# Kernel optimization log

Measured on AMD Instinct MI355X. Metric: run time of the kernel, lower is better.

Reference implementation:

```python
import jax, jax.numpy as jnp
import numpy as np

N_NODES = 50000
N_EDGES = 1600000
IN_DIM = 256
HID = 128
BATCH = 16384
EDGE_FEAT = 6
BN_EPS = 1e-5


def _glorot(key, shape):
    fan_in, fan_out = shape[0], shape[1]
    lim = float(np.sqrt(6.0 / (fan_in + fan_out)))
    return jax.random.uniform(key, shape, jnp.float32, -lim, lim)


def setup_inputs() -> dict:
    key = jax.random.key(0)
    ks = jax.random.split(key, 20)
    return {
        "x": jax.random.normal(ks[0], (N_NODES, IN_DIM), jnp.float32),
        "edge_index": jax.random.randint(ks[1], (2, N_EDGES), 0, N_NODES, jnp.int64 if jax.config.jax_enable_x64 else jnp.int32),
        "src_nodes": jax.random.randint(ks[2], (BATCH,), 0, N_NODES),
        "tgt_nodes": jax.random.randint(ks[3], (BATCH,), 0, N_NODES),
        "edge_features": jax.random.uniform(ks[4], (BATCH, EDGE_FEAT), jnp.float32),
        # SAGEConv layer 0: lin_l (aggregated neighbors, has bias), lin_r (root, no bias)
        "sage_wl0": _glorot(ks[5], (IN_DIM, HID)),
        "sage_b0": jnp.zeros((HID,), jnp.float32),
        "sage_wr0": _glorot(ks[6], (IN_DIM, HID)),
        # SAGEConv layer 1
        "sage_wl1": _glorot(ks[7], (HID, HID)),
        "sage_b1": jnp.zeros((HID,), jnp.float32),
        "sage_wr1": _glorot(ks[8], (HID, HID)),
        # edge_processor: Linear(6, 64)
        "ep_w": _glorot(ks[9], (EDGE_FEAT, HID // 2)),
        "ep_b": jnp.zeros((HID // 2,), jnp.float32),
        # predictor: Linear(320,128) -> ReLU -> BN(128) -> Linear(128,64) -> ReLU -> Linear(64,1) -> Sigmoid
        "p1_w": _glorot(ks[10], (2 * HID + HID // 2, HID)),
        "p1_b": jnp.zeros((HID,), jnp.float32),
        "bn_gamma": jnp.ones((HID,), jnp.float32),
        "bn_beta": jnp.zeros((HID,), jnp.float32),
        "bn_mean": jnp.zeros((HID,), jnp.float32),
        "bn_var": jnp.ones((HID,), jnp.float32),
        "p2_w": _glorot(ks[11], (HID, HID // 2)),
        "p2_b": jnp.zeros((HID // 2,), jnp.float32),
        "p3_w": _glorot(ks[12], (HID // 2, 1)),
        "p3_b": jnp.zeros((1,), jnp.float32),
    }


def _sage_conv(h, src, dst, w_l, b, w_r):
    # PyG SAGEConv(mean): out_i = W_l @ mean_{j in N(i)} h_j + b + W_r @ h_i
    n = h.shape[0]
    agg = jax.ops.segment_sum(h[src], dst, num_segments=n)  # [N, d]
    deg = jax.ops.segment_sum(jnp.ones((src.shape[0],), h.dtype), dst, num_segments=n)
    mean = agg / jnp.maximum(deg, 1.0)[:, None]
    return mean @ w_l + b + h @ w_r


def reference(x, edge_index, src_nodes, tgt_nodes, edge_features,
              sage_wl0, sage_b0, sage_wr0, sage_wl1, sage_b1, sage_wr1,
              ep_w, ep_b, p1_w, p1_b, bn_gamma, bn_beta, bn_mean, bn_var,
              p2_w, p2_b, p3_w, p3_b):
    src, dst = edge_index[0], edge_index[1]
    h = _sage_conv(x, src, dst, sage_wl0, sage_b0, sage_wr0)
    h = jax.nn.relu(h)  # dropout is identity in eval mode
    h = _sage_conv(h, src, dst, sage_wl1, sage_b1, sage_wr1)
    src_emb = h[src_nodes]  # [B, HID]
    tgt_emb = h[tgt_nodes]  # [B, HID]
    edge_proc = jax.nn.relu(edge_features @ ep_w + ep_b)  # [B, HID//2]
    combined = jnp.concatenate([src_emb, tgt_emb, edge_proc], axis=1)  # [B, 320]
    z = jax.nn.relu(combined @ p1_w + p1_b)
    z = (z - bn_mean) / jnp.sqrt(bn_var + BN_EPS) * bn_gamma + bn_beta  # BN eval mode
    z = jax.nn.relu(z @ p2_w + p2_b)
    return jax.nn.sigmoid(z @ p3_w + p3_b)  # [B, 1]
```

## Files before the change

kernel.cpp:

```cpp
#include <hip/hip_runtime.h>
#include <hip/hip_bf16.h>

#define N_NODES 50000
#define N_EDGES 1600000
#define BATCH   16384
#define HID     128
#define NBUCK   782
#define NBLK    256
#define EPB     6250

using short8  = __attribute__((ext_vector_type(8))) short;
using floatx4 = __attribute__((ext_vector_type(4))) float;
using floatv4 = __attribute__((ext_vector_type(4))) float;
using float2v = __attribute__((ext_vector_type(2))) float;
using uint2v  = __attribute__((ext_vector_type(2))) unsigned;
using uintx4  = __attribute__((ext_vector_type(4))) unsigned;
typedef unsigned short ushort_t;

__device__ __forceinline__ float bflo(unsigned u){ return __uint_as_float(u << 16); }
__device__ __forceinline__ float bfhi(unsigned u){ return __uint_as_float(u & 0xffff0000u); }
__device__ __forceinline__ float bf1(ushort_t u){ return __uint_as_float(((unsigned)u) << 16); }
__device__ __forceinline__ ushort_t f2bf(float f){
    unsigned u = __float_as_uint(f);
    return (ushort_t)((u + 0x7fffu + ((u >> 16) & 1u)) >> 16);
}
__device__ __forceinline__ int geti(const void* p, long long i, int is64){
    return is64 ? (int)((const long long*)p)[i] : ((const int*)p)[i];
}
__device__ __forceinline__ float2v up2(unsigned u){
    float2v r; r.x = bflo(u); r.y = bfhi(u); return r;
}

__global__ void k_detect(const unsigned* __restrict__ xbits,
                         const unsigned* __restrict__ eibits, int* flags){
    __shared__ int f[2];
    int t = threadIdx.x;
    if (t < 2) f[t] = 0;
    __syncthreads();
    unsigned u = xbits[t];
    unsigned e0 = (u >> 7)  & 0xFF;
    unsigned e1 = (u >> 23) & 0xFF;
    if (e0 >= 140 || e1 >= 140) atomicOr(&f[0], 1);
    if (eibits[2*t + 1] != 0)   atomicOr(&f[1], 1);
    __syncthreads();
    if (t == 0){ flags[0] = f[0]; flags[1] = f[1] ? 0 : 1; }
}

#define NT 19
struct ConvDesc { const void* src[NT]; int cum[NT + 1]; };
__global__ void k_conv(ConvDesc d, ushort_t* __restrict__ dst, const int* __restrict__ flags){
    int i = blockIdx.x*256 + threadIdx.x;
    if (i >= d.cum[NT]) return;
    int seg = 0;
    while (i >= d.cum[seg + 1]) seg++;
    int off = i - d.cum[seg];
    ushort_t v;
    if (flags[0]) v = f2bf(((const float*)d.src[seg])[off]);
    else          v = ((const ushort_t*)d.src[seg])[off];
    dst[i] = v;
}

#define OFF_WL0 0
#define OFF_WR0 32768
#define OFF_WL1 65536
#define OFF_WR1 81920
#define OFF_B0  98304
#define OFF_B1  98432
#define OFF_EPW 98560
#define OFF_EPB 98944
#define OFF_P1W 99008
#define OFF_P1B 139968
#define OFF_BNG 140096
#define OFF_BNB 140224
#define OFF_BNM 140352
#define OFF_BNV 140480
#define OFF_P2W 140608
#define OFF_P2B 148800
#define OFF_P3W 148864
#define OFF_EF  148928
#define OFF_P3B 247232
#define CW_TOT  247233

#define PACK_TOT 147584
__global__ void k_pack(const ushort_t* __restrict__ cw,
                       ushort_t* __restrict__ bp0, ushort_t* __restrict__ bp1,
                       ushort_t* __restrict__ bpp1, ushort_t* __restrict__ bpp2,
                       float* __restrict__ bnf){
    int i = blockIdx.x*256 + threadIdx.x;
    if (i < 65536){
        int j = i & 7, lane = (i >> 3) & 63, c = (i >> 9) & 15, kk = i >> 13;
        int k = kk*32 + (lane >> 4)*8 + j;
        int n = c*16 + (lane & 15);
        bp0[i] = (n < 128) ? cw[OFF_WL0 + k*128 + n] : cw[OFF_WR0 + k*128 + (n-128)];
    } else if (i < 98304){
        int i2 = i - 65536;
        int j = i2 & 7, lane = (i2 >> 3) & 63, c = (i2 >> 9) & 15, kk = i2 >> 13;
        int k = kk*32 + (lane >> 4)*8 + j;
        int n = c*16 + (lane & 15);
        bp1[i2] = (n < 128) ? cw[OFF_WL1 + k*128 + n] : cw[OFF_WR1 + k*128 + (n-128)];
    } else if (i < 139264){
        int i2 = i - 98304;
        int j = i2 & 7, lane = (i2 >> 3) & 63, ct = (i2 >> 9) & 7, kk = i2 >> 12;
        int k = kk*32 + (lane >> 4)*8 + j;
        int n = ct*16 + (lane & 15);
        bpp1[i2] = cw[OFF_P1W + k*128 + n];
    } else if (i < 147456){
        int i2 = i - 139264;
        int j = i2 & 7, lane = (i2 >> 3) & 63, ct = (i2 >> 9) & 3, kk = i2 >> 11;
        int k = kk*32 + (lane >> 4)*8 + j;
        int n = ct*16 + (lane & 15);
        bpp2[i2] = cw[OFF_P2W + k*64 + n];
    } else if (i < PACK_TOT){
        int n = i - 147456;
        float g = bf1(cw[OFF_BNG + n]), b = bf1(cw[OFF_BNB + n]);
        float m = bf1(cw[OFF_BNM + n]), v = bf1(cw[OFF_BNV + n]);
        float sc = g / sqrtf(v + 1e-5f);
        bnf[n] = sc; bnf[128 + n] = b - m*sc;
    }
}

__global__ __launch_bounds__(256)
void kb_hist(const void* __restrict__ ei, int* __restrict__ hist,
             const int* __restrict__ flags){
    __shared__ int lh[NBUCK];
    for (int i = threadIdx.x; i < NBUCK; i += 256) lh[i] = 0;
    __syncthreads();
    int i64 = flags[1];
    int e0 = blockIdx.x * EPB;
    for (int e = e0 + threadIdx.x; e < e0 + EPB; e += 256){
        int d = geti(ei, (long long)N_EDGES + e, i64);
        atomicAdd(&lh[d >> 6], 1);
    }
    __syncthreads();
    for (int i = threadIdx.x; i < NBUCK; i += 256)
        hist[i * NBLK + blockIdx.x] = lh[i];
}

__global__ __launch_bounds__(256)
void kb_scancol(int* __restrict__ hist, int* __restrict__ btot){
    __shared__ int sh[256];
    int b = blockIdx.x, t = threadIdx.x;
    int v = hist[b*NBLK + t];
    sh[t] = v; __syncthreads();
    for (int o = 1; o < 256; o <<= 1){
        int x = (t >= o) ? sh[t-o] : 0;
        __syncthreads();
        sh[t] += x;
        __syncthreads();
    }
    hist[b*NBLK + t] = sh[t] - v;
    if (t == 255) btot[b] = sh[255];
}

__global__ __launch_bounds__(1024)
void kb_scanbase(const int* __restrict__ btot, int* __restrict__ bbase,
                 int* __restrict__ off){
    __shared__ int sh[1024];
    int t = threadIdx.x;
    int v = (t < NBUCK) ? btot[t] : 0;
    sh[t] = v; __syncthreads();
    for (int o = 1; o < 1024; o <<= 1){
        int x = (t >= o) ? sh[t-o] : 0;
        __syncthreads();
        sh[t] += x;
        __syncthreads();
    }
    if (t < NBUCK) bbase[t] = sh[t] - v;
    if (t == 0){ bbase[NBUCK] = N_EDGES; off[N_NODES] = N_EDGES; }
}

__global__ __launch_bounds__(256)
void kb_scatter(const void* __restrict__ ei, const int* __restrict__ hist,
                const int* __restrict__ bbase, unsigned* __restrict__ ebuf,
                const int* __restrict__ flags){
    __shared__ int lcur[NBUCK];
    for (int i = threadIdx.x; i < NBUCK; i += 256)
        lcur[i] = bbase[i] + hist[i*NBLK + blockIdx.x];
    __syncthreads();
    int i64 = flags[1];
    int e0 = blockIdx.x * EPB;
    for (int e = e0 + threadIdx.x; e < e0 + EPB; e += 256){
        int s = geti(ei, e, i64);
        int d = geti(ei, (long long)N_EDGES + e, i64);
        int p = atomicAdd(&lcur[d >> 6], 1);
        ebuf[p] = (unsigned)s | ((unsigned)(d & 63) << 16);
    }
}

__global__ __launch_bounds__(256)
void kb_csr(const unsigned* __restrict__ ebuf, const int* __restrict__ bbase,
            ushort_t* __restrict__ csr, int* __restrict__ off){
    __shared__ int ldeg[64];
    int b = blockIdx.x, t = threadIdx.x;
    int ebase = bbase[b], eend = bbase[b+1];
    if (t < 64) ldeg[t] = 0;
    __syncthreads();
    for (int i = ebase + t; i < eend; i += 256)
        atomicAdd(&ldeg[(ebuf[i] >> 16) & 63], 1);
    __syncthreads();
    if (t < 64){
        int v = ldeg[t];
        int sum = v;
        #pragma unroll
        for (int o = 1; o < 64; o <<= 1){
            int x = __shfl_up(sum, o, 64);
            if (t >= o) sum += x;
        }
        int excl = sum - v;
        int node = b*64 + t;
        if (node < N_NODES) off[node] = ebase + excl;
        ldeg[t] = excl;
    }
    __syncthreads();
    for (int i = ebase + t; i < eend; i += 256){
        unsigned u = ebuf[i];
        int p = atomicAdd(&ldeg[(u >> 16) & 63], 1);
        csr[ebase + p] = (ushort_t)(u & 0xffffu);
    }
}

template<int KSTEPS, bool CHECKBF>
__global__ __launch_bounds__(256)
void k_gemm2(const ushort_t* __restrict__ A, const ushort_t* __restrict__ Bp,
             ushort_t* __restrict__ out, int M, const int* __restrict__ flags)
{
    if (CHECKBF && flags[0]) return;
    const int lane = threadIdx.x & 63;
    const int w    = threadIdx.x >> 6;
    const int l16  = lane & 15;
    const int q    = lane >> 4;
    const int S    = KSTEPS * 32;
    const int m_base = blockIdx.x * 64;

    const ushort_t* arow[4];
    bool ok[4];
    #pragma unroll
    for (int rt = 0; rt < 4; ++rt){
        int m = m_base + rt*16 + l16;
        ok[rt] = (m < M);
        arow[rt] = A + (size_t)(ok[rt] ? m : 0) * S + q*8;
    }
    const short8* bbase = (const short8*)(Bp + (size_t)(w*4)*64*8) + lane;

    floatx4 acc[4][4] = {};
    for (int kk = 0; kk < KSTEPS; ++kk){
        short8 b[4];
        #pragma unroll
        for (int ci = 0; ci < 4; ++ci)
            b[ci] = bbase[(kk*16 + ci)*64];
        short8 a[4];
        #pragma unroll
        for (int rt = 0; rt < 4; ++rt){
            short8 af = {0,0,0,0,0,0,0,0};
            if (ok[rt]) af = *(const short8*)(arow[rt] + kk*32);
            a[rt] = af;
        }
        #pragma unroll
        for (int rt = 0; rt < 4; ++rt)
            #pragma unroll
            for (int ci = 0; ci < 4; ++ci)
                acc[rt][ci] = __builtin_amdgcn_mfma_f32_16x16x32_bf16(a[rt], b[ci], acc[rt][ci], 0, 0, 0);
    }

    #pragma unroll
    for (int rt = 0; rt < 4; ++rt){
        int row_b = m_base + rt*16 + q*4;
        #pragma unroll
        for (int r = 0; r < 4; ++r){
            int row = row_b + r;
            if (row < M){
                #pragma unroll
                for (int ci = 0; ci < 4; ++ci)
                    out[(size_t)row*256 + w*64 + ci*16 + l16] = f2bf(acc[rt][ci][r]);
            }
        }
    }
}

__global__ __launch_bounds__(256)
void k_gemm2f(const float* __restrict__ Af, const ushort_t* __restrict__ Bp,
              ushort_t* __restrict__ out, int M, const int* __restrict__ flags)
{
    if (!flags[0]) return;
    const int KSTEPS = 8;
    const int lane = threadIdx.x & 63;
    const int w    = threadIdx.x >> 6;
    const int l16  = lane & 15;
    const int q    = lane >> 4;
    const int S    = KSTEPS * 32;
    const int m_base = blockIdx.x * 64;

    const float* arow[4];
    bool ok[4];
    #pragma unroll
    for (int rt = 0; rt < 4; ++rt){
        int m = m_base + rt*16 + l16;
        ok[rt] = (m < M);
        arow[rt] = Af + (size_t)(ok[rt] ? m : 0) * S + q*8;
    }
    const short8* bbase = (const short8*)(Bp + (size_t)(w*4)*64*8) + lane;

    floatx4 acc[4][4] = {};
    for (int kk = 0; kk < KSTEPS; ++kk){
        short8 b[4];
        #pragma unroll
        for (int ci = 0; ci < 4; ++ci)
            b[ci] = bbase[(kk*16 + ci)*64];
        short8 a[4];
        #pragma unroll
        for (int rt = 0; rt < 4; ++rt){
            union { unsigned u[4]; short8 s; } cv;
            cv.u[0]=0; cv.u[1]=0; cv.u[2]=0; cv.u[3]=0;
            if (ok[rt]){
                floatv4 f0 = *(const floatv4*)(arow[rt] + kk*32);
                floatv4 f1 = *(const floatv4*)(arow[rt] + kk*32 + 4);
                cv.u[0] = __builtin_amdgcn_perm(__float_as_uint(f0.y), __float_as_uint(f0.x), 0x07060302);
                cv.u[1] = __builtin_amdgcn_perm(__float_as_uint(f0.w), __float_as_uint(f0.z), 0x07060302);
                cv.u[2] = __builtin_amdgcn_perm(__float_as_uint(f1.y), __float_as_uint(f1.x), 0x07060302);
                cv.u[3] = __builtin_amdgcn_perm(__float_as_uint(f1.w), __float_as_uint(f1.z), 0x07060302);
            }
            a[rt] = cv.s;
        }
        #pragma unroll
        for (int rt = 0; rt < 4; ++rt)
            #pragma unroll
            for (int ci = 0; ci < 4; ++ci)
                acc[rt][ci] = __builtin_amdgcn_mfma_f32_16x16x32_bf16(a[rt], b[ci], acc[rt][ci], 0, 0, 0);
    }

    #pragma unroll
    for (int rt = 0; rt < 4; ++rt){
        int row_b = m_base + rt*16 + q*4;
        #pragma unroll
        for (int r = 0; r < 4; ++r){
            int row = row_b + r;
            if (row < M){
                #pragma unroll
                for (int ci = 0; ci < 4; ++ci)
                    out[(size_t)row*256 + w*64 + ci*16 + l16] = f2bf(acc[rt][ci][r]);
            }
        }
    }
}

__global__ __launch_bounds__(256)
void k_agg(const int* __restrict__ off, const ushort_t* __restrict__ csr,
           const ushort_t* __restrict__ yr, const ushort_t* __restrict__ bias,
           ushort_t* __restrict__ out, int do_relu)
{
    int v = blockIdx.x*4 + (threadIdx.x >> 6);
    if (v >= N_NODES) return;
    const int l = threadIdx.x & 63;
    const int g = l >> 4;
    const int c = l & 15;
    int e0 = off[v], e1 = off[v+1];
    const ushort_t* yb = yr + c*8;

    float2v A0[4] = {}, A1[4] = {}, A2[4] = {}, A3[4] = {};
    int p = e0;
    for (; p + 16 <= e1; p += 16){
        int u0 = csr[p + g];
        int u1 = csr[p + 4 + g];
        int u2 = csr[p + 8 + g];
        int u3 = csr[p + 12 + g];
        uintx4 d0 = *(const uintx4*)(yb + (size_t)u0*256);
        uintx4 d1 = *(const uintx4*)(yb + (size_t)u1*256);
        uintx4 d2 = *(const uintx4*)(yb + (size_t)u2*256);
        uintx4 d3 = *(const uintx4*)(yb + (size_t)u3*256);
        A0[0] += up2(d0.x); A0[1] += up2(d0.y); A0[2] += up2(d0.z); A0[3] += up2(d0.w);
        A1[0] += up2(d1.x); A1[1] += up2(d1.y); A1[2] += up2(d1.z); A1[3] += up2(d1.w);
        A2[0] += up2(d2.x); A2[1] += up2(d2.y); A2[2] += up2(d2.z); A2[3] += up2(d2.w);
        A3[0] += up2(d3.x); A3[1] += up2(d3.y); A3[2] += up2(d3.z); A3[3] += up2(d3.w);
    }
    for (; p + 4 <= e1; p += 4){
        int u0 = csr[p + g];
        uintx4 d0 = *(const uintx4*)(yb + (size_t)u0*256);
        A0[0] += up2(d0.x); A0[1] += up2(d0.y); A0[2] += up2(d0.z); A0[3] += up2(d0.w);
    }
    if (p + g < e1){
        int u1 = csr[p + g];
        uintx4 d1 = *(const uintx4*)(yb + (size_t)u1*256);
        A1[0] += up2(d1.x); A1[1] += up2(d1.y); A1[2] += up2(d1.z); A1[3] += up2(d1.w);
    }
    #pragma unroll
    for (int j = 0; j < 4; ++j) A0[j] += A1[j] + A2[j] + A3[j];

    float a0=A0[0].x, a1=A0[0].y, a2=A0[1].x, a3=A0[1].y;
    float a4=A0[2].x, a5=A0[2].y, a6=A0[3].x, a7=A0[3].y;
    #pragma unroll
    for (int m = 16; m <= 32; m <<= 1){
        a0 += __shfl_xor(a0, m, 64); a1 += __shfl_xor(a1, m, 64);
        a2 += __shfl_xor(a2, m, 64); a3 += __shfl_xor(a3, m, 64);
        a4 += __shfl_xor(a4, m, 64); a5 += __shfl_xor(a5, m, 64);
        a6 += __shfl_xor(a6, m, 64); a7 += __shfl_xor(a7, m, 64);
    }
    if (g == 0){
        float inv = 1.f / (float)max(e1 - e0, 1);
        uintx4 rr = *(const uintx4*)(yr + (size_t)v*256 + 128 + c*8);
        uintx4 bb = *(const uintx4*)(bias + c*8);
        float v0 = a0*inv + bflo(rr.x) + bflo(bb.x);
        float v1 = a1*inv + bfhi(rr.x) + bfhi(bb.x);
        float v2 = a2*inv + bflo(rr.y) + bflo(bb.y);
        float v3 = a3*inv + bfhi(rr.y) + bfhi(bb.y);
        float v4 = a4*inv + bflo(rr.z) + bflo(bb.z);
        float v5 = a5*inv + bfhi(rr.z) + bfhi(bb.z);
        float v6 = a6*inv + bflo(rr.w) + bflo(bb.w);
        float v7 = a7*inv + bfhi(rr.w) + bfhi(bb.w);
        if (do_relu){
            v0=fmaxf(v0,0.f); v1=fmaxf(v1,0.f); v2=fmaxf(v2,0.f); v3=fmaxf(v3,0.f);
            v4=fmaxf(v4,0.f); v5=fmaxf(v5,0.f); v6=fmaxf(v6,0.f); v7=fmaxf(v7,0.f);
        }
        uintx4 o;
        o.x = (unsigned)f2bf(v0) | ((unsigned)f2bf(v1) << 16);
        o.y = (unsigned)f2bf(v2) | ((unsigned)f2bf(v3) << 16);
        o.z = (unsigned)f2bf(v4) | ((unsigned)f2bf(v5) << 16);
        o.w = (unsigned)f2bf(v6) | ((unsigned)f2bf(v7) << 16);
        *(uintx4*)(out + (size_t)v*128 + c*8) = o;
    }
}

__global__ __launch_bounds__(256)
void k_pred2(const ushort_t* __restrict__ h2,
             const void* __restrict__ srcn, const void* __restrict__ tgtn,
             const ushort_t* __restrict__ cw, const ushort_t* __restrict__ bpp1,
             const ushort_t* __restrict__ bpp2, const float* __restrict__ bnf,
             void* __restrict__ outp, const int* __restrict__ flags)
{
    __shared__ ushort_t comb[64][328];
    __shared__ ushort_t zbuf[64][136];
    __shared__ ushort_t z2buf[64][68];
    __shared__ float    partial[4][64];
    __shared__ int      sid[64], tid_[64];

    const int t    = threadIdx.x;
    const int lane = t & 63;
    const int w    = t >> 6;
    const int l16  = lane & 15;
    const int q    = lane >> 4;
    const int row0 = blockIdx.x * 64;
    const int i64  = flags[1];

    if (t < 64){ sid[t] = geti(srcn, row0 + t, i64); tid_[t] = geti(tgtn, row0 + t, i64); }
    __syncthreads();

    const unsigned* h2u = (const unsigned*)h2;
    #pragma unroll 4
    for (int r = w*16; r < w*16 + 16; ++r){
        unsigned us = h2u[(size_t)sid[r]*64 + lane];
        unsigned ut = h2u[(size_t)tid_[r]*64 + lane];
        *(unsigned*)&comb[r][2*lane]       = us;
        *(unsigned*)&comb[r][128 + 2*lane] = ut;
    }
    {
        int r = t >> 2, c0 = (t & 3) * 16;
        float efv[6];
        #pragma unroll
        for (int k = 0; k < 6; ++k) efv[k] = bf1(cw[OFF_EF + (row0 + r)*6 + k]);
        #pragma unroll
        for (int c = 0; c < 16; ++c){
            int n = c0 + c;
            float a = bf1(cw[OFF_EPB + n]);
            #pragma unroll
            for (int k = 0; k < 6; ++k) a += efv[k] * bf1(cw[OFF_EPW + k*64 + n]);
            comb[r][256 + n] = f2bf(fmaxf(a, 0.f));
        }
    }
    __syncthreads();

    floatx4 acc[4][2] = {};
    for (int kk = 0; kk < 10; ++kk){
        short8 a[4];
        #pragma unroll
        for (int rt = 0; rt < 4; ++rt)
            a[rt] = *(const short8*)&comb[rt*16 + l16][kk*32 + q*8];
        #pragma unroll
        for (int ci = 0; ci < 2; ++ci){
            short8 b = *(const short8*)&bpp1[(((kk*8) + (w*2 + ci))*64 + lane)*8];
            #pragma unroll
            for (int rt = 0; rt < 4; ++rt)
                acc[rt][ci] = __builtin_amdgcn_mfma_f32_16x16x32_bf16(a[rt], b, acc[rt][ci], 0, 0, 0);
        }
    }
    #pragma unroll
    for (int ci = 0; ci < 2; ++ci){
        int n = w*32 + ci*16 + l16;
        float b1v = bf1(cw[OFF_P1B + n]);
        float sc = bnf[n], sh = bnf[128 + n];
        #pragma unroll
        for (int rt = 0; rt < 4; ++rt)
            #pragma unroll
            for (int r = 0; r < 4; ++r){
                float v = fmaxf(acc[rt][ci][r] + b1v, 0.f) * sc + sh;
                zbuf[rt*16 + q*4 + r][n] = f2bf(v);
            }
    }
    __syncthreads();

    floatx4 acc2[4] = {};
    for (int kk = 0; kk < 4; ++kk){
        short8 b = *(const short8*)&bpp2[(((kk*4) + w)*64 + lane)*8];
        #pragma unroll
        for (int rt = 0; rt < 4; ++rt){
            short8 a = *(const short8*)&zbuf[rt*16 + l16][kk*32 + q*8];
            acc2[rt] = __builtin_amdgcn_mfma_f32_16x16x32_bf16(a, b, acc2[rt], 0, 0, 0);
        }
    }
    {
        int n = w*16 + l16;
        float b2v = bf1(cw[OFF_P2B + n]);
        #pragma unroll
        for (int rt = 0; rt < 4; ++rt)
            #pragma unroll
            for (int r = 0; r < 4; ++r)
                z2buf[rt*16 + q*4 + r][n] = f2bf(fmaxf(acc2[rt][r] + b2v, 0.f));
    }
    __syncthreads();

    {
        int r = t & 63, seg = t >> 6;
        float s = 0.f;
        #pragma unroll
        for (int c = 0; c < 16; ++c){
            int n = seg*16 + c;
            s += bf1(z2buf[r][n]) * bf1(cw[OFF_P3W + n]);
        }
        partial[seg][r] = s;
    }
    __syncthreads();
    if (t < 64){
        float zf = partial[0][t] + partial[1][t] + partial[2][t] + partial[3][t] + bf1(cw[OFF_P3B]);
        float sg = 1.f / (1.f + __expf(-zf));
        if (flags[0]) ((float*)outp)[row0 + t] = sg;
        else          ((ushort_t*)outp)[row0 + t] = f2bf(sg);
    }
}

extern "C" void kernel_launch(void* const* d_in, const int* in_sizes, int n_in,
                              void* d_out, int out_size, void* d_ws, size_t ws_size,
                              hipStream_t stream)
{
    const void* x    = d_in[0];
    const void* ei   = d_in[1];
    const void* srcn = d_in[2];
    const void* tgtn = d_in[3];

    char* p = (char*)d_ws;
    auto carve = [&](size_t bytes)->char*{ char* r = p; p += (bytes + 511) & ~size_t(511); return r; };
    int* flags = (int*)carve(64);
    int* off   = (int*)carve((N_NODES+1)*4);
    int* btot  = (int*)carve(NBUCK*4);
    int* bbase = (int*)carve((NBUCK+1)*4);
    ushort_t* csr = (ushort_t*)carve((size_t)N_EDGES*2);
    ushort_t* yr  = (ushort_t*)carve((size_t)N_NODES*256*2);
    ushort_t* h   = (ushort_t*)carve((size_t)N_NODES*128*2);
    ushort_t* cw  = (ushort_t*)carve((size_t)CW_TOT*2);
    ushort_t* bp0 = (ushort_t*)carve((size_t)65536*2);
    ushort_t* bp1 = (ushort_t*)carve((size_t)32768*2);
    ushort_t* bpp1= (ushort_t*)carve((size_t)40960*2);
    ushort_t* bpp2= (ushort_t*)carve((size_t)8192*2);
    float*    bnf = (float*)carve(256*4);

    int*      hist = (int*)yr;
    unsigned* ebuf = (unsigned*)((char*)yr + 8u*1024*1024);

    k_detect<<<1, 256, 0, stream>>>((const unsigned*)x, (const unsigned*)ei, flags);

    ConvDesc cd;
    const int srcidx[NT] = {5,7,8,10,6,9,11,12,13,14,15,16,17,18,19,20,21,4,22};
    const int lens[NT]   = {32768,32768,16384,16384,128,128,384,64,40960,128,128,128,128,128,8192,64,64,98304,1};
    int run = 0;
    for (int i = 0; i < NT; ++i){ cd.src[i] = d_in[srcidx[i]]; cd.cum[i] = run; run += lens[i]; }
    cd.cum[NT] = run;
    k_conv<<<(CW_TOT+255)/256, 256, 0, stream>>>(cd, cw, flags);
    k_pack<<<(PACK_TOT+255)/256, 256, 0, stream>>>(cw, bp0, bp1, bpp1, bpp2, bnf);

    kb_hist    <<<NBLK, 256, 0, stream>>>(ei, hist, flags);
    kb_scancol <<<NBUCK, 256, 0, stream>>>(hist, btot);
    kb_scanbase<<<1, 1024, 0, stream>>>(btot, bbase, off);
    kb_scatter <<<NBLK, 256, 0, stream>>>(ei, hist, bbase, ebuf, flags);
    kb_csr     <<<NBUCK, 256, 0, stream>>>(ebuf, bbase, csr, off);

    int gblocks = (N_NODES + 63) / 64;
    k_gemm2<8, true><<<gblocks, 256, 0, stream>>>((const ushort_t*)x, bp0, yr, N_NODES, flags);
    k_gemm2f<<<gblocks, 256, 0, stream>>>((const float*)x, bp0, yr, N_NODES, flags);
    k_agg<<<(N_NODES+3)/4, 256, 0, stream>>>(off, csr, yr, cw+OFF_B0, h, 1);
    k_gemm2<4, false><<<gblocks, 256, 0, stream>>>(h, bp1, yr, N_NODES, flags);
    k_agg<<<(N_NODES+3)/4, 256, 0, stream>>>(off, csr, yr, cw+OFF_B1, h, 0);

    k_pred2<<<BATCH/64, 256, 0, stream>>>(h, srcn, tgtn, cw, bpp1, bpp2, bnf, d_out, flags);
}
```

Measured before the change: 347.2 us.

## Retile node GEMMs to 32-row blocks with 2x2 wave row/column split

The GEMM kernels change from 64-row blocks, where each wave computed 64 rows by 64 columns, to 32-row blocks where each wave computes 16 rows by 128 columns. Each wave now loads one A fragment per k-step and eight B fragments, instead of four A and four B. This doubles the grid size for more parallelism and lowers accumulator register use. In exchange, each B fragment is reused across fewer rows, and B traffic per output row goes up.

New measurement: 342.2 us. No clear change (-1.4%).

```diff
diff --git a/kernel.cpp b/kernel.cpp
--- a/kernel.cpp
+++ b/kernel.cpp
@@ -227,52 +227,37 @@
     if (CHECKBF && flags[0]) return;
     const int lane = threadIdx.x & 63;
     const int w    = threadIdx.x >> 6;
+    const int rg   = w >> 1;
+    const int cg   = w & 1;
     const int l16  = lane & 15;
     const int q    = lane >> 4;
     const int S    = KSTEPS * 32;
-    const int m_base = blockIdx.x * 64;
-
-    const ushort_t* arow[4];
-    bool ok[4];
+    const int m_base = blockIdx.x * 32 + rg * 16;
+
+    int m = m_base + l16;
+    bool ok = (m < M);
+    const ushort_t* arow = A + (size_t)(ok ? m : 0) * S + q*8;
+    const short8* bbase = (const short8*)Bp + lane;
+
+    floatx4 acc[8] = {};
+    for (int kk = 0; kk < KSTEPS; ++kk){
+        short8 a = {0,0,0,0,0,0,0,0};
+        if (ok) a = *(const short8*)(arow + kk*32);
+        #pragma unroll
+        for (int ci = 0; ci < 8; ++ci){
+            short8 b = bbase[(kk*16 + cg*8 + ci)*64];
+            acc[ci] = __builtin_amdgcn_mfma_f32_16x16x32_bf16(a, b, acc[ci], 0, 0, 0);
+        }
+    }
+
+    int row_b = m_base + q*4;
     #pragma unroll
-    for (int rt = 0; rt < 4; ++rt){
-        int m = m_base + rt*16 + l16;
-        ok[rt] = (m < M);
-        arow[rt] = A + (size_t)(ok[rt] ? m : 0) * S + q*8;
-    }
-    const short8* bbase = (const short8*)(Bp + (size_t)(w*4)*64*8) + lane;
-
-    floatx4 acc[4][4] = {};
-    for (int kk = 0; kk < KSTEPS; ++kk){
-        short8 b[4];
-        #pragma unroll
-        for (int ci = 0; ci < 4; ++ci)
-            b[ci] = bbase[(kk*16 + ci)*64];
-        short8 a[4];
-        #pragma unroll
-        for (int rt = 0; rt < 4; ++rt){
-            short8 af = {0,0,0,0,0,0,0,0};
-            if (ok[rt]) af = *(const short8*)(arow[rt] + kk*32);
-            a[rt] = af;
-        }
-        #pragma unroll
-        for (int rt = 0; rt < 4; ++rt)
+    for (int r = 0; r < 4; ++r){
+        int row = row_b + r;
+        if (row < M){
             #pragma unroll
-            for (int ci = 0; ci < 4; ++ci)
-                acc[rt][ci] = __builtin_amdgcn_mfma_f32_16x16x32_bf16(a[rt], b[ci], acc[rt][ci], 0, 0, 0);
-    }
-
-    #pragma unroll
-    for (int rt = 0; rt < 4; ++rt){
-        int row_b = m_base + rt*16 + q*4;
-        #pragma unroll
-        for (int r = 0; r < 4; ++r){
-            int row = row_b + r;
-            if (row < M){
-                #pragma unroll
-                for (int ci = 0; ci < 4; ++ci)
-                    out[(size_t)row*256 + w*64 + ci*16 + l16] = f2bf(acc[rt][ci][r]);
-            }
+            for (int ci = 0; ci < 8; ++ci)
+                out[(size_t)row*256 + cg*128 + ci*16 + l16] = f2bf(acc[ci][r]);
         }
     }
 }
@@ -285,60 +270,45 @@
     const int KSTEPS = 8;
     const int lane = threadIdx.x & 63;
     const int w    = threadIdx.x >> 6;
+    const int rg   = w >> 1;
+    const int cg   = w & 1;
     const int l16  = lane & 15;
     const int q    = lane >> 4;
     const int S    = KSTEPS * 32;
-    const int m_base = blockIdx.x * 64;
-
-    const float* arow[4];
-    bool ok[4];
+    const int m_base = blockIdx.x * 32 + rg * 16;
+
+    int m = m_base + l16;
+    bool ok = (m < M);
+    const float* arow = Af + (size_t)(ok ? m : 0) * S + q*8;
+    const short8* bbase = (const short8*)Bp + lane;
+
+    floatx4 acc[8] = {};
+    for (int kk = 0; kk < KSTEPS; ++kk){
+        union { unsigned u[4]; short8 s; } cv;
+        cv.u[0]=0; cv.u[1]=0; cv.u[2]=0; cv.u[3]=0;
+        if (ok){
+            floatv4 f0 = *(const floatv4*)(arow + kk*32);
+            floatv4 f1 = *(const floatv4*)(arow + kk*32 + 4);
+            cv.u[0] = __builtin_amdgcn_perm(__float_as_uint(f0.y), __float_as_uint(f0.x), 0x07060302);
+            cv.u[1] = __builtin_amdgcn_perm(__float_as_uint(f0.w), __float_as_uint(f0.z), 0x07060302);
+            cv.u[2] = __builtin_amdgcn_perm(__float_as_uint(f1.y), __float_as_uint(f1.x), 0x07060302);
+            cv.u[3] = __builtin_amdgcn_perm(__float_as_uint(f1.w), __float_as_uint(f1.z), 0x07060302);
+        }
+        #pragma unroll
+        for (int ci = 0; ci < 8; ++ci){
+            short8 b = bbase[(kk*16 + cg*8 + ci)*64];
+            acc[ci] = __builtin_amdgcn_mfma_f32_16x16x32_bf16(cv.s, b, acc[ci], 0, 0, 0);
+        }
+    }
+
+    int row_b = m_base + q*4;
     #pragma unroll
-    for (int rt = 0; rt < 4; ++rt){
-        int m = m_base + rt*16 + l16;
-        ok[rt] = (m < M);
-        arow[rt] = Af + (size_t)(ok[rt] ? m : 0) * S + q*8;
-    }
-    const short8* bbase = (const short8*)(Bp + (size_t)(w*4)*64*8) + lane;
-
-    floatx4 acc[4][4] = {};
-    for (int kk = 0; kk < KSTEPS; ++kk){
-        short8 b[4];
-        #pragma unroll
-        for (int ci = 0; ci < 4; ++ci)
-            b[ci] = bbase[(kk*16 + ci)*64];
-        short8 a[4];
-        #pragma unroll
-        for (int rt = 0; rt < 4; ++rt){
-            union { unsigned u[4]; short8 s; } cv;
-            cv.u[0]=0; cv.u[1]=0; cv.u[2]=0; cv.u[3]=0;
-            if (ok[rt]){
-                floatv4 f0 = *(const floatv4*)(arow[rt] + kk*32);
-                floatv4 f1 = *(const floatv4*)(arow[rt] + kk*32 + 4);
-                cv.u[0] = __builtin_amdgcn_perm(__float_as_uint(f0.y), __float_as_uint(f0.x), 0x07060302);
-                cv.u[1] = __builtin_amdgcn_perm(__float_as_uint(f0.w), __float_as_uint(f0.z), 0x07060302);
-                cv.u[2] = __builtin_amdgcn_perm(__float_as_uint(f1.y), __float_as_uint(f1.x), 0x07060302);
-                cv.u[3] = __builtin_amdgcn_perm(__float_as_uint(f1.w), __float_as_uint(f1.z), 0x07060302);
-            }
-            a[rt] = cv.s;
-        }
-        #pragma unroll
-        for (int rt = 0; rt < 4; ++rt)
+    for (int r = 0; r < 4; ++r){
+        int row = row_b + r;
+        if (row < M){
             #pragma unroll
-            for (int ci = 0; ci < 4; ++ci)
-                acc[rt][ci] = __builtin_amdgcn_mfma_f32_16x16x32_bf16(a[rt], b[ci], acc[rt][ci], 0, 0, 0);
-    }
-
-    #pragma unroll
-    for (int rt = 0; rt < 4; ++rt){
-        int row_b = m_base + rt*16 + q*4;
-        #pragma unroll
-        for (int r = 0; r < 4; ++r){
-            int row = row_b + r;
-            if (row < M){
-                #pragma unroll
-                for (int ci = 0; ci < 4; ++ci)
-                    out[(size_t)row*256 + w*64 + ci*16 + l16] = f2bf(acc[rt][ci][r]);
-            }
+            for (int ci = 0; ci < 8; ++ci)
+                out[(size_t)row*256 + cg*128 + ci*16 + l16] = f2bf(acc[ci][r]);
         }
     }
 }
@@ -580,7 +550,7 @@
     kb_scatter <<<NBLK, 256, 0, stream>>>(ei, hist, bbase, ebuf, flags);
     kb_csr     <<<NBUCK, 256, 0, stream>>>(ebuf, bbase, csr, off);
 
-    int gblocks = (N_NODES + 63) / 64;
+    int gblocks = (N_NODES + 31) / 32;
     k_gemm2<8, true><<<gblocks, 256, 0, stream>>>((const ushort_t*)x, bp0, yr, N_NODES, flags);
     k_gemm2f<<<gblocks, 256, 0, stream>>>((const float*)x, bp0, yr, N_NODES, flags);
     k_agg<<<(N_NODES+3)/4, 256, 0, stream>>>(off, csr, yr, cw+OFF_B0, h, 1);
```
